# Optimization experiments

Hardware: AMD Instinct MI355X
Metric: run time of the kernel (lower is better)

The kernel has to match this reference:

```python
import jax, jax.numpy as jnp
import numpy as np

B, N, DIM = 2, 2048, 512
HEADS, DIM_HEAD = 8, 64
INNER = HEADS * DIM_HEAD
SCALE = DIM_HEAD ** -0.5
ALPHA = 32.0 ** 2  # stable_softmax alpha


def setup_inputs() -> dict:
    key = jax.random.key(0)
    k1, k2, k3, k4 = jax.random.split(key, 4)
    x = jax.random.normal(k1, (B, N, DIM), dtype=jnp.float32)
    mask = jnp.ones((B, N), dtype=bool)
    # nn.Linear(dim, inner*3, bias=False) -> stored transposed for x @ W
    w_qkv = jax.random.normal(k2, (DIM, INNER * 3), dtype=jnp.float32) * (DIM ** -0.5)
    w_out = jax.random.normal(k3, (INNER, DIM), dtype=jnp.float32) * (INNER ** -0.5)
    b_out = jax.random.normal(k4, (DIM,), dtype=jnp.float32) * 0.01
    return {"x": x, "mask": mask, "w_qkv": w_qkv, "w_out": w_out, "b_out": b_out}


def stable_softmax(t, alpha=ALPHA):
    t = t / alpha
    t = t - jnp.max(t, axis=-1, keepdims=True)
    return jax.nn.softmax(t * alpha, axis=-1)


def reference(x, mask, w_qkv, w_out, b_out):
    b, n, _ = x.shape
    qkv = x @ w_qkv  # [b, n, 3*inner]
    q, k, v = jnp.split(qkv, 3, axis=-1)
    # 'b n (h d) -> b h n d'
    split_heads = lambda t: t.reshape(b, n, HEADS, DIM_HEAD).transpose(0, 2, 1, 3)
    q, k, v = split_heads(q), split_heads(k), split_heads(v)
    q = q * SCALE
    dots = jnp.einsum('bhid,bhjd->bhij', q, k)  # [b, h, n, n]
    mask_value = -jnp.finfo(dots.dtype).max
    # key padding mask: 'b j -> b 1 1 j'
    dots = jnp.where(mask[:, None, None, :], dots, mask_value)
    # causal mask: triu with offset j - i + 1 == 1 here
    causal = jnp.triu(jnp.ones((n, n), dtype=bool), k=1)
    dots = jnp.where(causal, mask_value, dots)
    attn = stable_softmax(dots)
    out = jnp.einsum('bhij,bhjd->bhid', attn, v)
    out = out.transpose(0, 2, 1, 3).reshape(b, n, INNER)  # 'b h n d -> b n (h d)'
    return out @ w_out + b_out
```

## Files before the change

kernel.cpp:

```cpp
#include <hip/hip_runtime.h>
#include <hip/hip_bf16.h>
#include <stdint.h>

#define B_ 2
#define N_ 2048
#define DIM_ 512
#define HEADS_ 8
#define DHEAD_ 64
#define INNER_ 512

typedef float f32x4 __attribute__((ext_vector_type(4)));
typedef float f32x16 __attribute__((ext_vector_type(16)));
typedef __bf16 bf16x8 __attribute__((ext_vector_type(8)));
typedef unsigned short us8 __attribute__((ext_vector_type(8)));
typedef unsigned int u32x4 __attribute__((ext_vector_type(4)));

static __device__ __forceinline__ unsigned short f2bf(float f) {
    union { float f; unsigned int u; } v; v.f = f;
    unsigned int r = v.u + 0x7fffu + ((v.u >> 16) & 1u);
    return (unsigned short)(r >> 16);
}

static __device__ __forceinline__ float exp2_fast(float x) {
    return __builtin_amdgcn_exp2f(x);
}

static __device__ __forceinline__ unsigned cvtpk(float lo, float hi) {
    unsigned r;
    asm("v_cvt_pk_bf16_f32 %0, %1, %2" : "=v"(r) : "v"(lo), "v"(hi));
    return r;
}

static __device__ __forceinline__ f32x4 mfma16(bf16x8 a, bf16x8 b, f32x4 c) {
    return __builtin_amdgcn_mfma_f32_16x16x32_bf16(a, b, c, 0, 0, 0);
}
static __device__ __forceinline__ f32x16 mfma32(bf16x8 a, bf16x8 b, f32x16 c) {
    return __builtin_amdgcn_mfma_f32_32x32x16_bf16(a, b, c, 0, 0, 0);
}

static __device__ __forceinline__ size_t qk_off(int bh, int n, int d) {
    int T = n >> 5, r = n & 31, c = d >> 4, s = d & 15;
    return ((((size_t)bh * 64 + T) * 4 + c) << 9) + (size_t)(((s >> 3) * 32 + r) * 8 + (s & 7));
}
static __device__ __forceinline__ size_t vt_off(int bh, int d, int n) {
    int tt = n >> 5, kk = n & 31, dblk = d >> 5, kc = (kk >> 4) & 1;
    int lane = (d & 31) + ((kk >> 3) & 1) * 32;
    return ((((size_t)bh * 64 + tt) * 2 + dblk) * 2 + kc) * 512 + (size_t)(lane * 8 + (kk & 7));
}

__global__ __launch_bounds__(256) void k_transpose_w(const float* __restrict__ in,
                                                     unsigned short* __restrict__ out,
                                                     int K, int N, int scale_cols,
                                                     float scale) {
    __shared__ float tile[32][33];
    const int tx = threadIdx.x & 31, ty = threadIdx.x >> 5;
    const int k0 = blockIdx.x * 32, n0 = blockIdx.y * 32;
#pragma unroll
    for (int j = 0; j < 4; j++)
        tile[ty + 8 * j][tx] = in[(size_t)(k0 + ty + 8 * j) * N + n0 + tx];
    __syncthreads();
#pragma unroll
    for (int j = 0; j < 4; j++) {
        int n = n0 + ty + 8 * j;
        float v = tile[tx][ty + 8 * j];
        if (n < scale_cols) v *= scale;
        out[(size_t)n * K + k0 + tx] = f2bf(v);
    }
}

template <int MODE>
__global__ __launch_bounds__(256) void k_gemm(const void* __restrict__ Av,
                                              const unsigned short* __restrict__ Bt,
                                              int K, int Ncols,
                                              float* __restrict__ Cf,
                                              const float* __restrict__ bias,
                                              unsigned short* __restrict__ Qb,
                                              unsigned short* __restrict__ Kb,
                                              unsigned short* __restrict__ Vt) {
    __shared__ unsigned short As[128 * 72];
    __shared__ unsigned short Bs[128 * 72];
    const int t = threadIdx.x;
    const int lane = t & 63;
    const int w = t >> 6;
    const int wy = w >> 1, wx = w & 1;
    const int lo = lane & 15, hi = lane >> 4;
    const int row0 = blockIdx.x * 128, col0 = blockIdx.y * 128;

    f32x4 acc[4][4];
#pragma unroll
    for (int m = 0; m < 4; m++)
#pragma unroll
        for (int n = 0; n < 4; n++) acc[m][n] = 0.f;

    for (int k0 = 0; k0 < K; k0 += 64) {
#pragma unroll
        for (int i = 0; i < 4; i++) {
            int chunk = t + i * 256;
            int r = chunk >> 3;
            int c = (chunk & 7) << 3;
            if (MODE == 0) {
                const float* Af = (const float*)Av;
                float4 v0 = *(const float4*)&Af[(size_t)(row0 + r) * K + k0 + c];
                float4 v1 = *(const float4*)&Af[(size_t)(row0 + r) * K + k0 + c + 4];
                us8 o;
                o[0] = f2bf(v0.x); o[1] = f2bf(v0.y); o[2] = f2bf(v0.z); o[3] = f2bf(v0.w);
                o[4] = f2bf(v1.x); o[5] = f2bf(v1.y); o[6] = f2bf(v1.z); o[7] = f2bf(v1.w);
                *(us8*)&As[r * 72 + c] = o;
            } else {
                const unsigned short* Ab = (const unsigned short*)Av;
                *(us8*)&As[r * 72 + c] = *(const us8*)&Ab[(size_t)(row0 + r) * K + k0 + c];
            }
            *(us8*)&Bs[r * 72 + c] = *(const us8*)&Bt[(size_t)(col0 + r) * K + k0 + c];
        }
        __syncthreads();
#pragma unroll
        for (int ks = 0; ks < 2; ks++) {
            bf16x8 af[4], bfr[4];
#pragma unroll
            for (int m = 0; m < 4; m++)
                af[m] = *(const bf16x8*)&As[(wy * 64 + m * 16 + lo) * 72 + ks * 32 + hi * 8];
#pragma unroll
            for (int n = 0; n < 4; n++)
                bfr[n] = *(const bf16x8*)&Bs[(wx * 64 + n * 16 + lo) * 72 + ks * 32 + hi * 8];
#pragma unroll
            for (int m = 0; m < 4; m++)
#pragma unroll
                for (int n = 0; n < 4; n++)
                    acc[m][n] = mfma16(af[m], bfr[n], acc[m][n]);
        }
        __syncthreads();
    }

#pragma unroll
    for (int m = 0; m < 4; m++) {
#pragma unroll
        for (int n = 0; n < 4; n++) {
#pragma unroll
            for (int r = 0; r < 4; r++) {
                int row = row0 + wy * 64 + m * 16 + hi * 4 + r;
                int col = col0 + wx * 64 + n * 16 + lo;
                float v = acc[m][n][r];
                if (MODE == 0) {
                    unsigned short bv = f2bf(v);
                    int b = row >> 11, nn = row & 2047;
                    int sec = col >> 9, cc = col & 511;
                    int h = cc >> 6, d = cc & 63;
                    int bh = b * HEADS_ + h;
                    if (sec == 0)      Qb[qk_off(bh, nn, d)] = bv;
                    else if (sec == 1) Kb[qk_off(bh, nn, d)] = bv;
                    else               Vt[vt_off(bh, d, nn)] = bv;
                } else {
                    Cf[(size_t)row * Ncols + col] = v + bias[col];
                }
            }
        }
    }
}


static __device__ __forceinline__ void pack_P(const f32x16& sT, int half,
                                              bf16x8& P0, bf16x8& P1) {
    unsigned X0 = cvtpk(sT[0], sT[1]),   X1 = cvtpk(sT[2], sT[3]);
    unsigned X2 = cvtpk(sT[4], sT[5]),   X3 = cvtpk(sT[6], sT[7]);
    unsigned Y0 = cvtpk(sT[8], sT[9]),   Y1 = cvtpk(sT[10], sT[11]);
    unsigned Y2 = cvtpk(sT[12], sT[13]), Y3 = cvtpk(sT[14], sT[15]);
    unsigned sx0 = __shfl_xor(X0, 32, 64), sx1 = __shfl_xor(X1, 32, 64);
    unsigned sx2 = __shfl_xor(X2, 32, 64), sx3 = __shfl_xor(X3, 32, 64);
    unsigned sy0 = __shfl_xor(Y0, 32, 64), sy1 = __shfl_xor(Y1, 32, 64);
    unsigned sy2 = __shfl_xor(Y2, 32, 64), sy3 = __shfl_xor(Y3, 32, 64);
    u32x4 pw0, pw1;
    pw0[0] = half ? sx2 : X0;
    pw0[1] = half ? sx3 : X1;
    pw0[2] = half ? X2 : sx0;
    pw0[3] = half ? X3 : sx1;
    pw1[0] = half ? sy2 : Y0;
    pw1[1] = half ? sy3 : Y1;
    pw1[2] = half ? Y2 : sy0;
    pw1[3] = half ? Y3 : sy1;
    P0 = __builtin_bit_cast(bf16x8, pw0);
    P1 = __builtin_bit_cast(bf16x8, pw1);
}

static __device__ __forceinline__ void do_tile(
    const unsigned short* kbase, const unsigned short* vbase, int tt,
    bool diag, int qg, int half,
    const bf16x8 (&qf)[4],
    float& m_, float& l_, f32x16& o0, f32x16& o1) {
    const unsigned short* kp = kbase + (size_t)tt * 2048;
    bf16x8 kf0 = *(const bf16x8*)(kp);
    bf16x8 kf1 = *(const bf16x8*)(kp + 512);
    bf16x8 kf2 = *(const bf16x8*)(kp + 1024);
    bf16x8 kf3 = *(const bf16x8*)(kp + 1536);
    const unsigned short* vp = vbase + (size_t)tt * 2048;
    bf16x8 vf00 = *(const bf16x8*)(vp);
    bf16x8 vf01 = *(const bf16x8*)(vp + 512);
    bf16x8 vf10 = *(const bf16x8*)(vp + 1024);
    bf16x8 vf11 = *(const bf16x8*)(vp + 1536);

    f32x16 sT = 0.f;
    sT = mfma32(kf0, qf[0], sT);
    sT = mfma32(kf1, qf[1], sT);
    sT = mfma32(kf2, qf[2], sT);
    sT = mfma32(kf3, qf[3], sT);

    if (diag) {
        const int kv0 = tt * 32;
#pragma unroll
        for (int r = 0; r < 16; r++) {
            int kv = kv0 + (r & 3) + 8 * (r >> 2) + 4 * half;
            if (kv > qg) sT[r] = -1e30f;
        }
    }

    float a0 = fmaxf(sT[0], sT[1]),  a1 = fmaxf(sT[2], sT[3]);
    float a2 = fmaxf(sT[4], sT[5]),  a3 = fmaxf(sT[6], sT[7]);
    float a4 = fmaxf(sT[8], sT[9]),  a5 = fmaxf(sT[10], sT[11]);
    float a6 = fmaxf(sT[12], sT[13]), a7 = fmaxf(sT[14], sT[15]);
    float mx = fmaxf(fmaxf(fmaxf(a0, a1), fmaxf(a2, a3)),
                     fmaxf(fmaxf(a4, a5), fmaxf(a6, a7)));
    mx = fmaxf(mx, __shfl_xor(mx, 32, 64));

    bool need = __any(mx > m_ + 11.f);
    float al = 1.f;
    if (need) {
        float mn = fmaxf(m_, mx);
        al = exp2_fast(m_ - mn);
        m_ = mn;
    }

#pragma unroll
    for (int r = 0; r < 16; r++) sT[r] = exp2_fast(sT[r] - m_);
    float b0 = sT[0] + sT[1],   b1 = sT[2] + sT[3];
    float b2 = sT[4] + sT[5],   b3 = sT[6] + sT[7];
    float b4 = sT[8] + sT[9],   b5 = sT[10] + sT[11];
    float b6 = sT[12] + sT[13], b7 = sT[14] + sT[15];
    float rs = ((b0 + b1) + (b2 + b3)) + ((b4 + b5) + (b6 + b7));
    rs += __shfl_xor(rs, 32, 64);
    if (need) {
        l_ = l_ * al + rs;
#pragma unroll
        for (int r = 0; r < 16; r++) { o0[r] *= al; o1[r] *= al; }
    } else {
        l_ += rs;
    }

    bf16x8 P0, P1;
    pack_P(sT, half, P0, P1);
    o0 = mfma32(vf00, P0, o0);
    o0 = mfma32(vf01, P1, o0);
    o1 = mfma32(vf10, P0, o1);
    o1 = mfma32(vf11, P1, o1);
}

static __device__ __forceinline__ void publish_merge(
    float (*Osh)[32 * 65], float (*Msh)[32], float (*Lsh)[32],
    int t, int w, int q31, int half, int bh, int q0,
    float m_, float l_, const f32x16& o0, const f32x16& o1,
    unsigned short* __restrict__ attb) {
    float* ow = Osh[w];
#pragma unroll
    for (int r = 0; r < 16; r++) {
        int d = (r & 3) + 8 * (r >> 2) + 4 * half;
        ow[q31 * 65 + d] = o0[r];
        ow[q31 * 65 + 32 + d] = o1[r];
    }
    if (half == 0) { Msh[w][q31] = m_; Lsh[w][q31] = l_; }
    __syncthreads();
    if (t < 256) {
        const int mq = t >> 3, d0 = (t & 7) * 8;
        float mg = -1e30f;
#pragma unroll
        for (int w2 = 0; w2 < 8; w2++) mg = fmaxf(mg, Msh[w2][mq]);
        float Lg = 0.f;
        float acc[8];
#pragma unroll
        for (int i = 0; i < 8; i++) acc[i] = 0.f;
#pragma unroll
        for (int w2 = 0; w2 < 8; w2++) {
            float f = exp2_fast(Msh[w2][mq] - mg);
            Lg += Lsh[w2][mq] * f;
#pragma unroll
            for (int i = 0; i < 8; i++) acc[i] += Osh[w2][mq * 65 + d0 + i] * f;
        }
        float inv = 1.f / Lg;
        us8 ov;
#pragma unroll
        for (int i = 0; i < 8; i++) ov[i] = f2bf(acc[i] * inv);
        const int b = bh >> 3, h = bh & 7;
        *(us8*)&attb[((size_t)b * N_ + q0 + mq) * INNER_ + h * DHEAD_ + d0] = ov;
    }
    __syncthreads();
}

__global__ __launch_bounds__(512, 4) void k_attn(const unsigned short* __restrict__ Qb,
                                                 const unsigned short* __restrict__ Kb,
                                                 const unsigned short* __restrict__ Vt,
                                                 unsigned short* __restrict__ attb) {
    __shared__ float Osh[8][32 * 65];
    __shared__ float Msh[8][32];
    __shared__ float Lsh[8][32];
    const int t = threadIdx.x, lane = t & 63, w = t >> 6;
    const int q31 = lane & 31, half = lane >> 5;

    int wg = (blockIdx.x & 7) * 64 + (blockIdx.x >> 3);
    const int bh = wg >> 5;
    const int pa = wg & 31;
    const int pb = 63 - pa;

    const unsigned short* kbase = Kb + (size_t)bh * 131072 + lane * 8;
    const unsigned short* vbase = Vt + (size_t)bh * 131072 + lane * 8;
    const unsigned short* qbh   = Qb + (size_t)bh * 131072 + lane * 8;

#pragma unroll
    for (int s = 0; s < 2; s++) {
        const int p = s ? pb : pa;
        const int q0 = p * 32, qg = q0 + q31;
        const unsigned short* qp = qbh + (size_t)p * 2048;
        bf16x8 qf[4];
        qf[0] = *(const bf16x8*)(qp);
        qf[1] = *(const bf16x8*)(qp + 512);
        qf[2] = *(const bf16x8*)(qp + 1024);
        qf[3] = *(const bf16x8*)(qp + 1536);
        float m_ = -1e30f, l_ = 0.f;
        f32x16 o0 = 0.f, o1 = 0.f;
        for (int tt = w; tt <= p; tt += 8)
            do_tile(kbase, vbase, tt, tt == p, qg, half, qf, m_, l_, o0, o1);
        publish_merge(Osh, Msh, Lsh, t, w, q31, half, bh, q0, m_, l_, o0, o1, attb);
    }
}

extern "C" void kernel_launch(void* const* d_in, const int* in_sizes, int n_in,
                              void* d_out, int out_size, void* d_ws, size_t ws_size,
                              hipStream_t stream) {
    const float* x     = (const float*)d_in[0];
    const float* w_qkv = (const float*)d_in[2];
    const float* w_out = (const float*)d_in[3];
    const float* b_out = (const float*)d_in[4];
    float* out = (float*)d_out;

    char* ws = (char*)d_ws;
    size_t off = 0;
    auto alloc = [&](size_t bytes) {
        void* p = ws + off;
        off += (bytes + 255) & ~(size_t)255;
        return p;
    };
    unsigned short* wqkvt = (unsigned short*)alloc((size_t)1536 * 512 * 2);
    unsigned short* woutt = (unsigned short*)alloc((size_t)512 * 512 * 2);
    unsigned short* Qb    = (unsigned short*)alloc((size_t)16 * 2048 * 64 * 2);
    unsigned short* Kb    = (unsigned short*)alloc((size_t)16 * 2048 * 64 * 2);
    unsigned short* Vt    = (unsigned short*)alloc((size_t)16 * 2048 * 64 * 2);
    unsigned short* attb  = (unsigned short*)alloc((size_t)4096 * 512 * 2);

    const float QSCALE = 0.125f * 1.44269504088896340736f;
    k_transpose_w<<<dim3(16, 48), 256, 0, stream>>>(w_qkv, wqkvt, 512, 1536, 512, QSCALE);
    k_transpose_w<<<dim3(16, 16), 256, 0, stream>>>(w_out, woutt, 512, 512, 0, 1.0f);
    k_gemm<0><<<dim3(32, 12), 256, 0, stream>>>(x, wqkvt, 512, 1536, nullptr, nullptr, Qb, Kb, Vt);
    k_attn<<<512, 512, 0, stream>>>(Qb, Kb, Vt, attb);
    k_gemm<1><<<dim3(32, 4), 256, 0, stream>>>(attb, woutt, 512, 512, out, b_out, nullptr, nullptr, nullptr);
}
```

Baseline: 64.32 us.

## Pre-cast x to bf16 and use direct global-to-LDS loads in GEMMs

```diff
diff --git a/kernel.cpp b/kernel.cpp
--- a/kernel.cpp
+++ b/kernel.cpp
@@ -38,6 +38,13 @@
     return __builtin_amdgcn_mfma_f32_32x32x16_bf16(a, b, c, 0, 0, 0);
 }
 
+static __device__ __forceinline__ void gl_lds16(const unsigned short* g, unsigned short* l) {
+    __builtin_amdgcn_global_load_lds(
+        (__attribute__((address_space(1))) void*)g,
+        (__attribute__((address_space(3))) void*)l,
+        16, 0, 0);
+}
+
 static __device__ __forceinline__ size_t qk_off(int bh, int n, int d) {
     int T = n >> 5, r = n & 31, c = d >> 4, s = d & 15;
     return ((((size_t)bh * 64 + T) * 4 + c) << 9) + (size_t)(((s >> 3) * 32 + r) * 8 + (s & 7));
@@ -46,6 +53,17 @@
     int tt = n >> 5, kk = n & 31, dblk = d >> 5, kc = (kk >> 4) & 1;
     int lane = (d & 31) + ((kk >> 3) & 1) * 32;
     return ((((size_t)bh * 64 + tt) * 2 + dblk) * 2 + kc) * 512 + (size_t)(lane * 8 + (kk & 7));
+}
+
+__global__ __launch_bounds__(256) void k_xcast(const float* __restrict__ in,
+                                               unsigned short* __restrict__ out) {
+    int idx = (blockIdx.x * 256 + threadIdx.x) * 8;
+    float4 v0 = *(const float4*)&in[idx];
+    float4 v1 = *(const float4*)&in[idx + 4];
+    us8 o;
+    o[0] = f2bf(v0.x); o[1] = f2bf(v0.y); o[2] = f2bf(v0.z); o[3] = f2bf(v0.w);
+    o[4] = f2bf(v1.x); o[5] = f2bf(v1.y); o[6] = f2bf(v1.z); o[7] = f2bf(v1.w);
+    *(us8*)&out[idx] = o;
 }
 
 __global__ __launch_bounds__(256) void k_transpose_w(const float* __restrict__ in,
@@ -69,7 +87,7 @@
 }
 
 template <int MODE>
-__global__ __launch_bounds__(256) void k_gemm(const void* __restrict__ Av,
+__global__ __launch_bounds__(256) void k_gemm(const unsigned short* __restrict__ A,
                                               const unsigned short* __restrict__ Bt,
                                               int K, int Ncols,
                                               float* __restrict__ Cf,
@@ -77,8 +95,8 @@
                                               unsigned short* __restrict__ Qb,
                                               unsigned short* __restrict__ Kb,
                                               unsigned short* __restrict__ Vt) {
-    __shared__ unsigned short As[128 * 72];
-    __shared__ unsigned short Bs[128 * 72];
+    __shared__ __align__(16) unsigned short As[128 * 64];
+    __shared__ __align__(16) unsigned short Bs[128 * 64];
     const int t = threadIdx.x;
     const int lane = t & 63;
     const int w = t >> 6;
@@ -86,6 +104,9 @@
     const int lo = lane & 15, hi = lane >> 4;
     const int row0 = blockIdx.x * 128, col0 = blockIdx.y * 128;
 
+    const int lr = lane >> 3;
+    const int lc = (lane & 7) * 8;
+
     f32x4 acc[4][4];
 #pragma unroll
     for (int m = 0; m < 4; m++)
@@ -95,22 +116,10 @@
     for (int k0 = 0; k0 < K; k0 += 64) {
 #pragma unroll
         for (int i = 0; i < 4; i++) {
-            int chunk = t + i * 256;
-            int r = chunk >> 3;
-            int c = (chunk & 7) << 3;
-            if (MODE == 0) {
-                const float* Af = (const float*)Av;
-                float4 v0 = *(const float4*)&Af[(size_t)(row0 + r) * K + k0 + c];
-                float4 v1 = *(const float4*)&Af[(size_t)(row0 + r) * K + k0 + c + 4];
-                us8 o;
-                o[0] = f2bf(v0.x); o[1] = f2bf(v0.y); o[2] = f2bf(v0.z); o[3] = f2bf(v0.w);
-                o[4] = f2bf(v1.x); o[5] = f2bf(v1.y); o[6] = f2bf(v1.z); o[7] = f2bf(v1.w);
-                *(us8*)&As[r * 72 + c] = o;
-            } else {
-                const unsigned short* Ab = (const unsigned short*)Av;
-                *(us8*)&As[r * 72 + c] = *(const us8*)&Ab[(size_t)(row0 + r) * K + k0 + c];
-            }
-            *(us8*)&Bs[r * 72 + c] = *(const us8*)&Bt[(size_t)(col0 + r) * K + k0 + c];
+            int seg = w * 4 + i;
+            int r = seg * 8 + lr;
+            gl_lds16(&A [(size_t)(row0 + r) * K + k0 + lc], &As[seg * 512]);
+            gl_lds16(&Bt[(size_t)(col0 + r) * K + k0 + lc], &Bs[seg * 512]);
         }
         __syncthreads();
 #pragma unroll
@@ -118,10 +127,10 @@
             bf16x8 af[4], bfr[4];
 #pragma unroll
             for (int m = 0; m < 4; m++)
-                af[m] = *(const bf16x8*)&As[(wy * 64 + m * 16 + lo) * 72 + ks * 32 + hi * 8];
+                af[m] = *(const bf16x8*)&As[(wy * 64 + m * 16 + lo) * 64 + ks * 32 + hi * 8];
 #pragma unroll
             for (int n = 0; n < 4; n++)
-                bfr[n] = *(const bf16x8*)&Bs[(wx * 64 + n * 16 + lo) * 72 + ks * 32 + hi * 8];
+                bfr[n] = *(const bf16x8*)&Bs[(wx * 64 + n * 16 + lo) * 64 + ks * 32 + hi * 8];
 #pragma unroll
             for (int m = 0; m < 4; m++)
 #pragma unroll
@@ -347,15 +356,17 @@
     };
     unsigned short* wqkvt = (unsigned short*)alloc((size_t)1536 * 512 * 2);
     unsigned short* woutt = (unsigned short*)alloc((size_t)512 * 512 * 2);
+    unsigned short* xb    = (unsigned short*)alloc((size_t)4096 * 512 * 2);
     unsigned short* Qb    = (unsigned short*)alloc((size_t)16 * 2048 * 64 * 2);
     unsigned short* Kb    = (unsigned short*)alloc((size_t)16 * 2048 * 64 * 2);
     unsigned short* Vt    = (unsigned short*)alloc((size_t)16 * 2048 * 64 * 2);
     unsigned short* attb  = (unsigned short*)alloc((size_t)4096 * 512 * 2);
 
     const float QSCALE = 0.125f * 1.44269504088896340736f;
+    k_xcast<<<1024, 256, 0, stream>>>(x, xb);
     k_transpose_w<<<dim3(16, 48), 256, 0, stream>>>(w_qkv, wqkvt, 512, 1536, 512, QSCALE);
     k_transpose_w<<<dim3(16, 16), 256, 0, stream>>>(w_out, woutt, 512, 512, 0, 1.0f);
-    k_gemm<0><<<dim3(32, 12), 256, 0, stream>>>(x, wqkvt, 512, 1536, nullptr, nullptr, Qb, Kb, Vt);
+    k_gemm<0><<<dim3(32, 12), 256, 0, stream>>>(xb, wqkvt, 512, 1536, nullptr, nullptr, Qb, Kb, Vt);
     k_attn<<<512, 512, 0, stream>>>(Qb, Kb, Vt, attb);
     k_gemm<1><<<dim3(32, 4), 256, 0, stream>>>(attb, woutt, 512, 512, out, b_out, nullptr, nullptr, nullptr);
 }
```

Measured after the change: 67.37 us. 1.05x slower.

## Merge two query-pair groups per 1024-thread block with halved LDS merge buffer

Applied to the files above, without the earlier changes.

```diff
diff --git a/kernel.cpp b/kernel.cpp
--- a/kernel.cpp
+++ b/kernel.cpp
@@ -13,6 +13,7 @@
 typedef float f32x16 __attribute__((ext_vector_type(16)));
 typedef __bf16 bf16x8 __attribute__((ext_vector_type(8)));
 typedef unsigned short us8 __attribute__((ext_vector_type(8)));
+typedef unsigned short us4 __attribute__((ext_vector_type(4)));
 typedef unsigned int u32x4 __attribute__((ext_vector_type(4)));
 
 static __device__ __forceinline__ unsigned short f2bf(float f) {
@@ -252,60 +253,25 @@
     o1 = mfma32(vf11, P1, o1);
 }
 
-static __device__ __forceinline__ void publish_merge(
-    float (*Osh)[32 * 65], float (*Msh)[32], float (*Lsh)[32],
-    int t, int w, int q31, int half, int bh, int q0,
-    float m_, float l_, const f32x16& o0, const f32x16& o1,
-    unsigned short* __restrict__ attb) {
-    float* ow = Osh[w];
-#pragma unroll
-    for (int r = 0; r < 16; r++) {
-        int d = (r & 3) + 8 * (r >> 2) + 4 * half;
-        ow[q31 * 65 + d] = o0[r];
-        ow[q31 * 65 + 32 + d] = o1[r];
-    }
-    if (half == 0) { Msh[w][q31] = m_; Lsh[w][q31] = l_; }
-    __syncthreads();
-    if (t < 256) {
-        const int mq = t >> 3, d0 = (t & 7) * 8;
-        float mg = -1e30f;
-#pragma unroll
-        for (int w2 = 0; w2 < 8; w2++) mg = fmaxf(mg, Msh[w2][mq]);
-        float Lg = 0.f;
-        float acc[8];
-#pragma unroll
-        for (int i = 0; i < 8; i++) acc[i] = 0.f;
-#pragma unroll
-        for (int w2 = 0; w2 < 8; w2++) {
-            float f = exp2_fast(Msh[w2][mq] - mg);
-            Lg += Lsh[w2][mq] * f;
-#pragma unroll
-            for (int i = 0; i < 8; i++) acc[i] += Osh[w2][mq * 65 + d0 + i] * f;
-        }
-        float inv = 1.f / Lg;
-        us8 ov;
-#pragma unroll
-        for (int i = 0; i < 8; i++) ov[i] = f2bf(acc[i] * inv);
-        const int b = bh >> 3, h = bh & 7;
-        *(us8*)&attb[((size_t)b * N_ + q0 + mq) * INNER_ + h * DHEAD_ + d0] = ov;
-    }
-    __syncthreads();
-}
-
-__global__ __launch_bounds__(512, 4) void k_attn(const unsigned short* __restrict__ Qb,
-                                                 const unsigned short* __restrict__ Kb,
-                                                 const unsigned short* __restrict__ Vt,
-                                                 unsigned short* __restrict__ attb) {
-    __shared__ float Osh[8][32 * 65];
-    __shared__ float Msh[8][32];
-    __shared__ float Lsh[8][32];
+__global__ __launch_bounds__(1024, 8) void k_attn(const unsigned short* __restrict__ Qb,
+                                                  const unsigned short* __restrict__ Kb,
+                                                  const unsigned short* __restrict__ Vt,
+                                                  unsigned short* __restrict__ attb) {
+    __shared__ float Osh[16][32 * 33];
+    __shared__ float Msh[16][32];
+    __shared__ float Lsh[16][32];
     const int t = threadIdx.x, lane = t & 63, w = t >> 6;
+    const int g = w >> 3;
+    const int w8 = w & 7;
     const int q31 = lane & 31, half = lane >> 5;
-
-    int wg = (blockIdx.x & 7) * 64 + (blockIdx.x >> 3);
-    const int bh = wg >> 5;
-    const int pa = wg & 31;
-    const int pb = 63 - pa;
+    const int tl = t & 511;
+
+    int wg = (blockIdx.x & 7) * 32 + (blockIdx.x >> 3);
+    const int bh = wg >> 4;
+    const int jp = wg & 15;
+    const int pi = jp * 2 + g;
+    const int pa = pi, pb = 63 - pi;
+    const int b = bh >> 3, h = bh & 7;
 
     const unsigned short* kbase = Kb + (size_t)bh * 131072 + lane * 8;
     const unsigned short* vbase = Vt + (size_t)bh * 131072 + lane * 8;
@@ -323,9 +289,60 @@
         qf[3] = *(const bf16x8*)(qp + 1536);
         float m_ = -1e30f, l_ = 0.f;
         f32x16 o0 = 0.f, o1 = 0.f;
-        for (int tt = w; tt <= p; tt += 8)
+        for (int tt = w8; tt <= p; tt += 8)
             do_tile(kbase, vbase, tt, tt == p, qg, half, qf, m_, l_, o0, o1);
-        publish_merge(Osh, Msh, Lsh, t, w, q31, half, bh, q0, m_, l_, o0, o1, attb);
+
+        float* ow = Osh[w];
+#pragma unroll
+        for (int r = 0; r < 16; r++) {
+            int d = (r & 3) + 8 * (r >> 2) + 4 * half;
+            ow[q31 * 33 + d] = o0[r];
+        }
+        if (half == 0) { Msh[w][q31] = m_; Lsh[w][q31] = l_; }
+        __syncthreads();
+
+        float mg = -1e30f, inv = 0.f;
+        int mq = tl >> 3, d0 = (tl & 7) * 4;
+        if (tl < 256) {
+#pragma unroll
+            for (int w2 = 0; w2 < 8; w2++) mg = fmaxf(mg, Msh[g * 8 + w2][mq]);
+            float Lg = 0.f;
+            float acc[4] = {0.f, 0.f, 0.f, 0.f};
+#pragma unroll
+            for (int w2 = 0; w2 < 8; w2++) {
+                float f = exp2_fast(Msh[g * 8 + w2][mq] - mg);
+                Lg += Lsh[g * 8 + w2][mq] * f;
+#pragma unroll
+                for (int i = 0; i < 4; i++) acc[i] += Osh[g * 8 + w2][mq * 33 + d0 + i] * f;
+            }
+            inv = 1.f / Lg;
+            us4 ov;
+#pragma unroll
+            for (int i = 0; i < 4; i++) ov[i] = f2bf(acc[i] * inv);
+            *(us4*)&attb[((size_t)b * N_ + q0 + mq) * INNER_ + h * DHEAD_ + d0] = ov;
+        }
+        __syncthreads();
+
+#pragma unroll
+        for (int r = 0; r < 16; r++) {
+            int d = (r & 3) + 8 * (r >> 2) + 4 * half;
+            ow[q31 * 33 + d] = o1[r];
+        }
+        __syncthreads();
+        if (tl < 256) {
+            float acc[4] = {0.f, 0.f, 0.f, 0.f};
+#pragma unroll
+            for (int w2 = 0; w2 < 8; w2++) {
+                float f = exp2_fast(Msh[g * 8 + w2][mq] - mg);
+#pragma unroll
+                for (int i = 0; i < 4; i++) acc[i] += Osh[g * 8 + w2][mq * 33 + d0 + i] * f;
+            }
+            us4 ov;
+#pragma unroll
+            for (int i = 0; i < 4; i++) ov[i] = f2bf(acc[i] * inv);
+            *(us4*)&attb[((size_t)b * N_ + q0 + mq) * INNER_ + h * DHEAD_ + 32 + d0] = ov;
+        }
+        __syncthreads();
     }
 }
 
@@ -356,6 +373,6 @@
     k_transpose_w<<<dim3(16, 48), 256, 0, stream>>>(w_qkv, wqkvt, 512, 1536, 512, QSCALE);
     k_transpose_w<<<dim3(16, 16), 256, 0, stream>>>(w_out, woutt, 512, 512, 0, 1.0f);
     k_gemm<0><<<dim3(32, 12), 256, 0, stream>>>(x, wqkvt, 512, 1536, nullptr, nullptr, Qb, Kb, Vt);
-    k_attn<<<512, 512, 0, stream>>>(Qb, Kb, Vt, attb);
+    k_attn<<<256, 1024, 0, stream>>>(Qb, Kb, Vt, attb);
     k_gemm<1><<<dim3(32, 4), 256, 0, stream>>>(attb, woutt, 512, 512, out, b_out, nullptr, nullptr, nullptr);
 }
```

New measurement: 176.8 us. 2.75x slower.
